# Kernel tuning notes

Measured on AMD Instinct MI355X. Metric: run time of the kernel, lower is better.

Reference implementation:

```python
import jax, jax.numpy as jnp
import numpy as np

J = 8          # number of octaves
Q = 8          # wavelets per octave (first order)
T = 16384      # signal length (power of two)
B = 4          # batch size
XI_MAX = 0.35  # center frequency of the mother wavelet (cycles/sample)


def _filters():
    """Frequency-domain Morlet-like analytic filterbank + Gaussian lowpass."""
    om = np.arange(T) / T                                   # normalized freqs in [0,1)
    # first-order: J*Q log-spaced analytic bandpass filters
    k1 = np.arange(J * Q)
    xi1 = XI_MAX * 2.0 ** (-k1 / Q)                         # (N1,) center freqs
    sig1 = xi1 * (2.0 ** (1.0 / Q) - 1.0)                   # ~1/Q-octave bandwidth
    psi1 = np.exp(-((om[None, :] - xi1[:, None]) ** 2) / (2.0 * sig1[:, None] ** 2))
    # second-order: J octave-spaced (Q2=1) wider filters
    k2 = np.arange(J).astype(np.float64)
    xi2 = XI_MAX * 2.0 ** (-k2)                             # (N2,)
    sig2 = xi2 * 0.5                                        # octave bandwidth
    psi2 = np.exp(-((om[None, :] - xi2[:, None]) ** 2) / (2.0 * sig2[:, None] ** 2))
    # lowpass phi at scale 2^J (symmetric on the circle)
    d = np.minimum(om, 1.0 - om)
    sig_phi = XI_MAX * 2.0 ** (-J)
    phi = np.exp(-(d ** 2) / (2.0 * sig_phi ** 2))
    # valid second-order paths: xi2 < xi1 (equivalent of j2 > j1)
    mask = (xi2[None, :] < xi1[:, None])                    # (N1, N2) bool
    return (jnp.asarray(psi1, jnp.float32), jnp.asarray(psi2, jnp.float32),
            jnp.asarray(phi, jnp.float32), jnp.asarray(mask))


def setup_inputs() -> dict:
    key = jax.random.key(0)
    x = jax.random.normal(key, (B, 1, T), dtype=jnp.float32)
    psi1_hat, psi2_hat, phi_hat, mask = _filters()
    return {"x": x, "psi1_hat": psi1_hat, "psi2_hat": psi2_hat,
            "phi_hat": phi_hat, "mask": mask, "stride": 2 ** J}


def reference(x, psi1_hat, psi2_hat, phi_hat, mask, stride):
    # x: (B,1,T); psi1_hat: (N1,T); psi2_hat: (N2,T); phi_hat: (T,); mask: (N1,N2)
    X = jnp.fft.fft(x)                                       # (B,1,T) complex
    lp = lambda h: jnp.real(jnp.fft.ifft(h * phi_hat))[..., ::stride]  # lowpass + subsample
    # zeroth order
    S0 = lp(X)[:, :, None, :]                                # (B,1,1,T')
    # first order: bandpass -> modulus
    U1 = jnp.abs(jnp.fft.ifft(X[:, :, None, :] * psi1_hat))  # (B,1,N1,T)
    U1h = jnp.fft.fft(U1)
    S1 = lp(U1h)                                             # (B,1,N1,T')
    # second order: bandpass the first-order envelopes -> modulus
    U2 = jnp.abs(jnp.fft.ifft(U1h[:, :, :, None, :] * psi2_hat))  # (B,1,N1,N2,T)
    S2 = lp(jnp.fft.fft(U2)) * mask[None, None, :, :, None]  # (B,1,N1,N2,T')
    b, c, n1, n2, tp = S2.shape
    S2 = S2.reshape(b, c, n1 * n2, tp)
    Sx = jnp.concatenate([S0, S1, S2], axis=2)               # (B,C=1,P,T')
    # torch module: (B,C,T,F) -> (B,1,T,F*C); with C=1 this is the identity reshape
    return Sx.reshape(b, 1, Sx.shape[2], Sx.shape[3] * c)
```

## Files before the change

kernel.cpp:

```cpp
#include <hip/hip_runtime.h>
#include <math.h>

#define T_LEN   16384
#define NTH     512
#define TPRIME  64
#define NPATH   577
#define INV_T   (1.0f/16384.0f)
#define TWO_PI  6.28318530717958647692f
#define NW      640
#define NH      (NW + 1)
#define C8C     0.92387953251128675613f
#define C8S     0.38268343236508977173f

__device__ __forceinline__ int rev4(int i) {
    int r = 0;
#pragma unroll
    for (int p = 0; p < 7; ++p) { r = (r << 2) | (i & 3); i >>= 2; }
    return r;
}
__device__ __forceinline__ int IDX(int i) {
    return i ^ ((i >> 4) & 15) ^ ((i >> 8) & 15);
}
#define S6 IDX
__device__ __forceinline__ int UIDX(int n) {
    return n ^ ((n >> 5) & 31) ^ ((n >> 10) & 31);
}
__device__ __forceinline__ int US(int n) { return n ^ ((n >> 5) & 31); }

__device__ __forceinline__ void inv_bf4(float2& A0, float2& A1, float2& A2, float2& A3,
                                        float c1, float s1) {
    float sr = A0.x + A1.x + A2.x + A3.x, si = A0.y + A1.y + A2.y + A3.y;
    float tr = A0.x - A1.y - A2.x + A3.y, ti = A0.y + A1.x - A2.y - A3.x;
    float ur = A0.x - A1.x + A2.x - A3.x, ui = A0.y - A1.y + A2.y - A3.y;
    float vr = A0.x + A1.y - A2.x - A3.y, vi = A0.y - A1.x - A2.y + A3.x;
    float c2 = c1*c1 - s1*s1, s2 = 2.f*c1*s1;
    float c3 = c1*c2 - s1*s2, s3 = c1*s2 + s1*c2;
    A0 = make_float2(sr, si);
    A1 = make_float2(tr*c1 - ti*s1, tr*s1 + ti*c1);
    A2 = make_float2(ur*c2 - ui*s2, ur*s2 + ui*c2);
    A3 = make_float2(vr*c3 - vi*s3, vr*s3 + vi*c3);
}
__device__ __forceinline__ void fwd_bf4(float2& B0, float2& B1, float2& B2, float2& B3,
                                        float c1, float s1) {
    float c2 = c1*c1 - s1*s1, s2 = 2.f*c1*s1;
    float c3 = c1*c2 - s1*s2, s3 = c1*s2 + s1*c2;
    float trr = B1.x*c1 + B1.y*s1, tii = B1.y*c1 - B1.x*s1;
    float urr = B2.x*c2 + B2.y*s2, uii = B2.y*c2 - B2.x*s2;
    float vrr = B3.x*c3 + B3.y*s3, vii = B3.y*c3 - B3.x*s3;
    float s0r = B0.x, s0i = B0.y;
    B0 = make_float2(s0r + trr + urr + vrr, s0i + tii + uii + vii);
    B1 = make_float2(s0r + tii - urr - vii, s0i - trr - uii + vrr);
    B2 = make_float2(s0r - trr + urr - vrr, s0i - tii + uii - vii);
    B3 = make_float2(s0r - tii - urr + vii, s0i + trr - uii - vrr);
}

template<int Q>
__device__ __forceinline__ void inv_group16(float2* v, int jp) {
    float a0 = (float)jp * (TWO_PI / (float)(4 * Q));
    float cw, sw; __sincosf(a0, &sw, &cw);
    float c = cw, s = sw;
#pragma unroll
    for (int rp = 0; rp < 4; ++rp) {
        inv_bf4(v[rp], v[4+rp], v[8+rp], v[12+rp], c, s);
        float cn = c*C8C - s*C8S, sn = c*C8S + s*C8C;
        c = cn; s = sn;
    }
    float b0 = (float)jp * (TWO_PI / (float)Q);
    float cb, sb; __sincosf(b0, &sb, &cb);
#pragma unroll
    for (int r = 0; r < 4; ++r)
        inv_bf4(v[4*r], v[4*r+1], v[4*r+2], v[4*r+3], cb, sb);
}
template<int QA>
__device__ __forceinline__ void fwd_group16(float2* v, int jp) {
    float aA = (float)jp * (TWO_PI / (float)(4 * QA));
    float cA, sA; __sincosf(aA, &sA, &cA);
#pragma unroll
    for (int r = 0; r < 4; ++r)
        fwd_bf4(v[4*r], v[4*r+1], v[4*r+2], v[4*r+3], cA, sA);
    float aB = (float)jp * (TWO_PI / (float)(16 * QA));
    float cB, sB; __sincosf(aB, &sB, &cB);
    float c = cB, s = sB;
#pragma unroll
    for (int rp = 0; rp < 4; ++rp) {
        fwd_bf4(v[rp], v[4+rp], v[8+rp], v[12+rp], c, s);
        float cn = c*C8C - s*C8S, sn = c*C8S + s*C8C;
        c = cn; s = sn;
    }
}

template<int LQ>
__device__ void inv_pass16(float2* buf) {
    const int q = 1 << LQ, qp = q >> 2;
    __syncthreads();
#pragma unroll
    for (int it = 0; it < 2; ++it) {
        int g2 = threadIdx.x + it * NTH;
        int jp = g2 & (qp - 1);
        int base = ((g2 >> (LQ - 2)) << (LQ + 2)) | jp;
        float2 v[16];
#pragma unroll
        for (int r = 0; r < 4; ++r)
#pragma unroll
            for (int rp = 0; rp < 4; ++rp)
                v[4*r+rp] = buf[IDX(base + r*q + rp*qp)];
        inv_group16<(1 << LQ)>(v, jp);
#pragma unroll
        for (int r = 0; r < 4; ++r)
#pragma unroll
            for (int rp = 0; rp < 4; ++rp)
                buf[IDX(base + r*q + rp*qp)] = v[4*r+rp];
    }
}

__device__ void inv_pass16_g(const float2* __restrict__ src, const float* __restrict__ filt,
                             float2* buf, int clo, int chi) {
#pragma unroll 1
    for (int it = 0; it < 2; ++it) {
        int jp = threadIdx.x + it * NTH;
        float2 v[16];
#pragma unroll
        for (int r = 0; r < 4; ++r)
#pragma unroll
            for (int rp = 0; rp < 4; ++rp) {
                int ch = 4*r + rp;
                if (ch >= clo && ch <= chi) {
                    int i = jp + r*4096 + rp*1024;
                    float2 a = src[i]; float p = filt[i];
                    v[4*r+rp] = make_float2(a.x*p, a.y*p);
                } else {
                    v[4*r+rp] = make_float2(0.f, 0.f);
                }
            }
        inv_group16<4096>(v, jp);
#pragma unroll
        for (int r = 0; r < 4; ++r)
#pragma unroll
            for (int rp = 0; rp < 4; ++rp)
                buf[IDX(jp + r*4096 + rp*1024)] = v[4*r+rp];
        asm volatile("" ::: "memory");
    }
}

__device__ void mod_fwd4(float2* buf) {
    __syncthreads();
#pragma unroll
    for (int it = 0; it < 8; ++it) {
        int base = (threadIdx.x + it * NTH) << 2;
        float2 a0 = buf[IDX(base)], a1 = buf[IDX(base+1)], a2 = buf[IDX(base+2)], a3 = buf[IDX(base+3)];
        inv_bf4(a0, a1, a2, a3, 1.0f, 0.0f);
        float2 b0 = make_float2(sqrtf(a0.x*a0.x + a0.y*a0.y) * INV_T, 0.f);
        float2 b1 = make_float2(sqrtf(a1.x*a1.x + a1.y*a1.y) * INV_T, 0.f);
        float2 b2 = make_float2(sqrtf(a2.x*a2.x + a2.y*a2.y) * INV_T, 0.f);
        float2 b3 = make_float2(sqrtf(a3.x*a3.x + a3.y*a3.y) * INV_T, 0.f);
        fwd_bf4(b0, b1, b2, b3, 1.0f, 0.0f);
        buf[IDX(base)] = b0; buf[IDX(base+1)] = b1; buf[IDX(base+2)] = b2; buf[IDX(base+3)] = b3;
    }
}

template<int LQA>
__device__ void fwd_pass16(float2* buf) {
    const int qA = 1 << LQA, qB = 4 * qA;
    __syncthreads();
#pragma unroll
    for (int it = 0; it < 2; ++it) {
        int g2 = threadIdx.x + it * NTH;
        int jp = g2 & (qA - 1);
        int base = ((g2 >> LQA) << (LQA + 4)) | jp;
        float2 v[16];
#pragma unroll
        for (int r = 0; r < 4; ++r)
#pragma unroll
            for (int rp = 0; rp < 4; ++rp)
                v[4*r+rp] = buf[IDX(base + r*qB + rp*qA)];
        fwd_group16<(1 << LQA)>(v, jp);
#pragma unroll
        for (int r = 0; r < 4; ++r)
#pragma unroll
            for (int rp = 0; rp < 4; ++rp)
                buf[IDX(base + r*qB + rp*qA)] = v[4*r+rp];
    }
}

__device__ void fwd_last_store_zs(float2* buf, float2* __restrict__ gout, int nchunks,
                                  float2* zs) {
    __syncthreads();
#pragma unroll 1
    for (int it = 0; it < 2; ++it) {
        int jp = threadIdx.x + it * NTH;
        float2 v[16];
#pragma unroll
        for (int r = 0; r < 4; ++r)
#pragma unroll
            for (int rp = 0; rp < 4; ++rp)
                v[4*r+rp] = buf[IDX(jp + r*4096 + rp*1024)];
        fwd_group16<1024>(v, jp);
        if (it == 0 && jp < 124) zs[jp] = v[0];
#pragma unroll
        for (int r = 0; r < 4; ++r)
#pragma unroll
            for (int rp = 0; rp < 4; ++rp) {
                int ch = 4*r + rp;
                if (ch < nchunks)
                    gout[jp + r*4096 + rp*1024] = v[4*r+rp];
            }
        asm volatile("" ::: "memory");
    }
}

__global__ __launch_bounds__(512) void k1_prep(const float* __restrict__ x,
                                               const float* __restrict__ phi,
                                               float2* __restrict__ Z,
                                               float* __restrict__ hws,
                                               int B2) {
    const int bi = blockIdx.x;
    if (bi < B2) {
        const int b = bi >> 1;
        const int jp = ((bi & 1) << 9) | threadIdx.x;
        const float* xb = x + (size_t)b * T_LEN;
        float2* Zb = Z + (size_t)b * T_LEN;
        float2 v[16];
#pragma unroll
        for (int r = 0; r < 4; ++r)
#pragma unroll
            for (int rp = 0; rp < 4; ++rp)
                v[4*r+rp] = make_float2(xb[jp + r*4096 + rp*1024], 0.f);
        inv_group16<4096>(v, jp);
#pragma unroll
        for (int r = 0; r < 4; ++r)
#pragma unroll
            for (int rp = 0; rp < 4; ++rp)
                Zb[jp + r*4096 + rp*1024] = v[4*r+rp];
    } else {
        const int d = (bi - B2) * 8 + (threadIdx.x >> 6);
        const int l = threadIdx.x & 63;
        float p = 0.f;
#pragma unroll
        for (int j = 0; j < 8; ++j) {
            int w = l + 64 * j;
            int k = (w < 256) ? w : (15872 + w);
            int r = (k * d) & (T_LEN - 1);
            p += phi[k] * __cosf((float)r * (TWO_PI / (float)T_LEN));
        }
        p += __shfl_xor(p, 1);  p += __shfl_xor(p, 2);  p += __shfl_xor(p, 4);
        p += __shfl_xor(p, 8);  p += __shfl_xor(p, 16); p += __shfl_xor(p, 32);
        if (l == 0 && d <= NW) hws[d] = p * INV_T;
    }
}

__global__ __launch_bounds__(256) void k2_chunk_s0(const float2* __restrict__ Z,
                                                   const float* __restrict__ x,
                                                   const float* __restrict__ hws,
                                                   float2* __restrict__ wsX,
                                                   float* __restrict__ out,
                                                   int B4) {
    __shared__ float2 lds[4096];
    __shared__ float hl[NH];
    const int bi = blockIdx.x;
    if (bi < B4) {
        const int b = bi >> 2;
        const int c0 = (bi & 3) << 12;
        const float2* Zb = Z + (size_t)b * T_LEN + c0;
        for (int i = threadIdx.x; i < 4096; i += 256) lds[IDX(i)] = Zb[i];
        {
            __syncthreads();
            int g = threadIdx.x;
            int jp = g & 63, base = ((g >> 6) << 10) | jp;
            float2 v[16];
#pragma unroll
            for (int r = 0; r < 4; ++r)
#pragma unroll
                for (int rp = 0; rp < 4; ++rp)
                    v[4*r+rp] = lds[IDX(base + r*256 + rp*64)];
            inv_group16<256>(v, jp);
#pragma unroll
            for (int r = 0; r < 4; ++r)
#pragma unroll
                for (int rp = 0; rp < 4; ++rp)
                    lds[IDX(base + r*256 + rp*64)] = v[4*r+rp];
        }
        {
            __syncthreads();
            int g = threadIdx.x;
            int jp = g & 3, base = ((g >> 2) << 6) | jp;
            float2 v[16];
#pragma unroll
            for (int r = 0; r < 4; ++r)
#pragma unroll
                for (int rp = 0; rp < 4; ++rp)
                    v[4*r+rp] = lds[IDX(base + r*16 + rp*4)];
            inv_group16<16>(v, jp);
#pragma unroll
            for (int r = 0; r < 4; ++r)
#pragma unroll
                for (int rp = 0; rp < 4; ++rp)
                    lds[IDX(base + r*16 + rp*4)] = v[4*r+rp];
        }
        __syncthreads();
        float2* W = wsX + (size_t)b * T_LEN;
#pragma unroll
        for (int it = 0; it < 4; ++it) {
            int bl = (threadIdx.x + it * 256) << 2;
            float2 a0 = lds[IDX(bl)], a1 = lds[IDX(bl+1)], a2 = lds[IDX(bl+2)], a3 = lds[IDX(bl+3)];
            inv_bf4(a0, a1, a2, a3, 1.0f, 0.0f);
            int rb = rev4(c0 + bl);
            W[rb]         = make_float2(a0.x, -a0.y);
            W[rb + 4096]  = make_float2(a1.x, -a1.y);
            W[rb + 8192]  = make_float2(a2.x, -a2.y);
            W[rb + 12288] = make_float2(a3.x, -a3.y);
        }
    } else {
        const int q = bi - B4;
        const int b = q >> 3;
        const int m0 = (q & 7) << 3;
        for (int i = threadIdx.x; i < NH; i += 256) hl[i] = hws[i];
        __syncthreads();
        const float* xb = x + (size_t)b * T_LEN;
        const int m = m0 + (threadIdx.x >> 5);
        const int s = threadIdx.x & 31;
        const int c = m << 8;
        float acc = 0.f;
        for (int e = -NW + s; e <= NW; e += 32) {
            int n = (c + e) & (T_LEN - 1);
            int a = e < 0 ? -e : e;
            acc += hl[a] * xb[n];
        }
        acc += __shfl_xor(acc, 1);  acc += __shfl_xor(acc, 2);
        acc += __shfl_xor(acc, 4);  acc += __shfl_xor(acc, 8);
        acc += __shfl_xor(acc, 16);
        if (s == 0) out[(size_t)b * (NPATH * TPRIME) + m] = acc;
    }
}

__global__ __launch_bounds__(NTH)
__attribute__((amdgpu_waves_per_eu(1, 2)))
void pass_b(const float2* __restrict__ wsX,
            const float* __restrict__ psi1,
            const float* __restrict__ phi,
            float2* __restrict__ wsU,
            float* __restrict__ out) {
    __shared__ float2 buf[T_LEN];
    __shared__ float2 zs[128];
    const int blk = blockIdx.x;
    const int b = blk >> 6, n1 = blk & 63;
    float xi1T = 5734.4f * exp2f(-(float)n1 / 8.0f);
    int clo = (int)(0.40f * xi1T) >> 10;
    int chi = ((int)(1.60f * xi1T)) >> 10; if (chi > 15) chi = 15;
    inv_pass16_g(wsX + (size_t)b * T_LEN, psi1 + (size_t)n1 * T_LEN, buf, clo, chi);
    inv_pass16<8>(buf);
    inv_pass16<4>(buf);
    mod_fwd4(buf);
    fwd_pass16<2>(buf);
    fwd_pass16<6>(buf);
    const int n2min = (n1 >> 3) + 1;
    int nch = 0;
    if (n2min <= 7) {
        int S = 24084 >> n2min;
        nch = (S >> 10) + 1; if (nch > 10) nch = 10;
    }
    fwd_last_store_zs(buf, wsU + (size_t)blk * T_LEN, nch, zs);
    __syncthreads();
    const int m = threadIdx.x >> 3;
    const int s = threadIdx.x & 7;
    float acc = 0.f;
    for (int k = 1 + s; k < 124; k += 8) {
        float ph = phi[k];
        float2 z = zs[k];
        float ang = (float)((k * m) & 63) * (TWO_PI / 64.0f);
        float sn, cs; __sincosf(ang, &sn, &cs);
        acc += 2.0f * ph * (z.x * cs - z.y * sn);
    }
    acc += __shfl_xor(acc, 1);
    acc += __shfl_xor(acc, 2);
    acc += __shfl_xor(acc, 4);
    if (s == 0) {
        acc += zs[0].x * phi[0];
        out[(size_t)b * (NPATH * TPRIME) + (size_t)(1 + n1) * TPRIME + m] = acc * INV_T;
    }
}

__global__ __launch_bounds__(256) void k4_med_zero(const float2* __restrict__ wsU,
                                                   const float* __restrict__ psi2,
                                                   const float* __restrict__ hws,
                                                   float* __restrict__ out) {
    __shared__ float2 sc[4096];
    __shared__ float u8s[8192];
    __shared__ float h2s[321];
    const int tj = threadIdx.x;
    const int idx = blockIdx.x % 312, b = blockIdx.x / 312;

    if (idx >= 24) {
        int z = idx - 24;
        int g = 0, cum = 0;
#pragma unroll
        for (int gg = 0; gg < 8; ++gg) {
            int c = 8 * (gg + 1);
            if (z >= cum + c) { cum += c; g = gg + 1; }
        }
        int zz = z - cum;
        int n1 = g * 8 + zz / (g + 1);
        int n2 = zz % (g + 1);
        if (tj < TPRIME)
            out[(size_t)b * (NPATH * TPRIME) + (size_t)(65 + (n1 << 3) + n2) * TPRIME + tj] = 0.f;
        return;
    }

    const int n2 = (idx < 8) ? 1 : 2;
    const int n1 = (idx < 8) ? idx : idx - 8;
    for (int i = tj; i < 321; i += 256) h2s[i] = 2.0f * hws[2 * i];
    const float2* Ub = wsU + (size_t)((b << 6) | n1) * T_LEN;
    const float* p2 = psi2 + (size_t)n2 * T_LEN;
    const int lim = (n2 == 1) ? 10240 : 6144;
#pragma unroll 1
    for (int h = 0; h < 2; ++h) {
        float2 v[16];
#pragma unroll
        for (int r = 0; r < 4; ++r) {
#pragma unroll
            for (int rp = 0; rp < 4; ++rp) {
                int i = tj + r*1024 + rp*256;
                float2 y0 = Ub[i]; float q0 = p2[i];
                float ar = y0.x * q0, ai = y0.y * q0;
                if (i + 4096 < lim) {
                    float2 y1 = Ub[i + 4096]; float q1 = p2[i + 4096];
                    if (h == 0) { ar += y1.x*q1; ai += y1.y*q1; }
                    else        { ar -= y1.x*q1; ai -= y1.y*q1; }
                }
                if (i + 8192 < lim) {
                    float2 y2 = Ub[i + 8192]; float q2 = p2[i + 8192];
                    ar += y2.x*q2; ai += y2.y*q2;
                }
                if (h == 1) {
                    float ang = (float)i * (TWO_PI / 8192.0f);
                    float sn, cs; __sincosf(ang, &sn, &cs);
                    float nr = ar*cs - ai*sn, ni = ar*sn + ai*cs;
                    ar = nr; ai = ni;
                }
                v[4*r+rp] = make_float2(ar, ai);
            }
            asm volatile("" ::: "memory");
        }
        inv_group16<1024>(v, tj);
#pragma unroll
        for (int r = 0; r < 4; ++r)
#pragma unroll
            for (int rp = 0; rp < 4; ++rp)
                sc[S6(tj + r*1024 + rp*256)] = v[4*r+rp];
        __syncthreads();
        {
            int jp = tj & 15, base = ((tj >> 4) << 8) | jp;
#pragma unroll
            for (int r = 0; r < 4; ++r)
#pragma unroll
                for (int rp = 0; rp < 4; ++rp)
                    v[4*r+rp] = sc[S6(base + r*64 + rp*16)];
            inv_group16<64>(v, jp);
#pragma unroll
            for (int r = 0; r < 4; ++r)
#pragma unroll
                for (int rp = 0; rp < 4; ++rp)
                    sc[S6(base + r*64 + rp*16)] = v[4*r+rp];
        }
        __syncthreads();
        float mg[16];
        {
            int base = tj << 4;
#pragma unroll
            for (int r = 0; r < 4; ++r)
#pragma unroll
                for (int rp = 0; rp < 4; ++rp)
                    v[4*r+rp] = sc[S6(base + 4*r + rp)];
            inv_group16<4>(v, 0);
#pragma unroll
            for (int k = 0; k < 16; ++k)
                mg[k] = sqrtf(v[k].x*v[k].x + v[k].y*v[k].y) * INV_T;
        }
        __syncthreads();
        int rt = ((tj & 3) << 6) | (((tj >> 2) & 3) << 4) | (((tj >> 4) & 3) << 2) | (tj >> 6);
#pragma unroll
        for (int r = 0; r < 4; ++r)
#pragma unroll
            for (int rp = 0; rp < 4; ++rp)
                u8s[UIDX(2 * (rp*1024 + r*256 + rt) + h)] = mg[4*r+rp];
    }
    __syncthreads();
    const int m = tj >> 2, s = tj & 3;
    float acc = 0.f;
    for (int e = -320 + s; e <= 320; e += 4) {
        int n = (128*m + e) & 8191;
        int a = e < 0 ? -e : e;
        acc += h2s[a] * u8s[UIDX(n)];
    }
    acc += __shfl_xor(acc, 1);
    acc += __shfl_xor(acc, 2);
    if (s == 0)
        out[(size_t)b * (NPATH * TPRIME) + (size_t)(65 + (n1 << 3) + n2) * TPRIME + m] = acc;
}

__global__ __launch_bounds__(256) void k4_small(const float2* __restrict__ wsU,
                                                const float* __restrict__ psi2,
                                                const float* __restrict__ hws,
                                                float* __restrict__ out) {
    __shared__ float2 buf[4096];
    __shared__ float hd[161];
    const int t = threadIdx.x;
    const int p = blockIdx.x % 200, b = blockIdx.x / 200;
    int n1, n2;
    if      (p < 24)  { n2 = 3; n1 = p; }
    else if (p < 56)  { n2 = 4; n1 = p - 24; }
    else if (p < 96)  { n2 = 5; n1 = p - 56; }
    else if (p < 144) { n2 = 6; n1 = p - 96; }
    else              { n2 = 7; n1 = p - 144; }
    if (t < 161) hd[t] = 4.0f * hws[4 * t];
    const int kc = ((((int)(24084.0f * exp2f(-(float)n2))) >> 10) + 1) << 2;
    const float2* Ub = wsU + (size_t)((b << 6) | n1) * T_LEN;
    const float* p2 = psi2 + (size_t)n2 * T_LEN;
    float2 v[16];
#pragma unroll
    for (int r = 0; r < 4; ++r)
#pragma unroll
        for (int rp = 0; rp < 4; ++rp) {
            int ch = 4*r + rp;
            if (ch < kc) {
                int i = t + r*1024 + rp*256;
                float2 u = Ub[i]; float pp = p2[i];
                v[4*r+rp] = make_float2(u.x*pp, u.y*pp);
            } else {
                v[4*r+rp] = make_float2(0.f, 0.f);
            }
        }
    inv_group16<1024>(v, t);
#pragma unroll
    for (int r = 0; r < 4; ++r)
#pragma unroll
        for (int rp = 0; rp < 4; ++rp)
            buf[S6(t + r*1024 + rp*256)] = v[4*r+rp];
    __syncthreads();
    {
        int jp = t & 15, base = ((t >> 4) << 8) | jp;
#pragma unroll
        for (int r = 0; r < 4; ++r)
#pragma unroll
            for (int rp = 0; rp < 4; ++rp)
                v[4*r+rp] = buf[S6(base + r*64 + rp*16)];
        inv_group16<64>(v, jp);
#pragma unroll
        for (int r = 0; r < 4; ++r)
#pragma unroll
            for (int rp = 0; rp < 4; ++rp)
                buf[S6(base + r*64 + rp*16)] = v[4*r+rp];
    }
    __syncthreads();
    float mg[16];
    {
        int base = t << 4;
#pragma unroll
        for (int r = 0; r < 4; ++r)
#pragma unroll
            for (int rp = 0; rp < 4; ++rp)
                v[4*r+rp] = buf[S6(base + 4*r + rp)];
        inv_group16<4>(v, 0);
#pragma unroll
        for (int k = 0; k < 16; ++k)
            mg[k] = sqrtf(v[k].x*v[k].x + v[k].y*v[k].y) * INV_T;
    }
    __syncthreads();
    float* uf = (float*)buf;
    int rt = ((t & 3) << 6) | (((t >> 2) & 3) << 4) | (((t >> 4) & 3) << 2) | (t >> 6);
#pragma unroll
    for (int r = 0; r < 4; ++r)
#pragma unroll
        for (int rp = 0; rp < 4; ++rp)
            uf[US(rp*1024 + r*256 + rt)] = mg[4*r+rp];
    __syncthreads();
    const int m = t >> 2, s = t & 3;
    float acc = 0.f;
    for (int e = -160 + s; e <= 160; e += 4) {
        int n = (64*m + e) & 4095;
        int a = e < 0 ? -e : e;
        acc += hd[a] * uf[US(n)];
    }
    acc += __shfl_xor(acc, 1);
    acc += __shfl_xor(acc, 2);
    if (s == 0)
        out[(size_t)b * (NPATH * TPRIME) + (size_t)(65 + (n1 << 3) + n2) * TPRIME + m] = acc;
}

extern "C" void kernel_launch(void* const* d_in, const int* in_sizes, int n_in,
                              void* d_out, int out_size, void* d_ws, size_t ws_size,
                              hipStream_t stream) {
    const float* x    = (const float*)d_in[0];
    const float* psi1 = (const float*)d_in[1];
    const float* psi2 = (const float*)d_in[2];
    const float* phi  = (const float*)d_in[3];
    float* out = (float*)d_out;

    const int B = in_sizes[0] / T_LEN;

    float*  hws = (float*)d_ws;
    float2* wsX = (float2*)((char*)d_ws + 4096);
    float2* wsU = (float2*)((char*)d_ws + 4096 + (size_t)B * T_LEN * sizeof(float2));
    float2* Z   = wsU;

    k1_prep<<<2 * B + 81, 512, 0, stream>>>(x, phi, Z, hws, 2 * B);
    k2_chunk_s0<<<4 * B + 8 * B, 256, 0, stream>>>(Z, x, hws, wsX, out, 4 * B);
    pass_b<<<B * 64, NTH, 0, stream>>>(wsX, psi1, phi, wsU, out);
    k4_med_zero<<<B * 312, 256, 0, stream>>>(wsU, psi2, hws, out);
    k4_small<<<B * 200, 256, 0, stream>>>(wsU, psi2, hws, out);
}
```

Measured before the change: 103.4 us.

## Run both half-transforms of medium paths concurrently and move zero-fill into small kernel

The medium second-order kernel now uses 512 threads per block, with two 256-thread halves computing the even and odd half-size inverse FFTs in parallel instead of looping over them sequentially. Both halves share one 64 KB shared buffer that is reused for the envelope before the lowpass reduction, which is now split eight ways per output. The zero-fill of masked-out paths is moved from the medium kernel into the small-path kernel, so the medium launch only has its 24 working blocks per batch. This aims to shorten the critical path of the few long medium blocks, at the cost of more shared memory per block and lower occupancy.

```diff
diff --git a/kernel.cpp b/kernel.cpp
--- a/kernel.cpp
+++ b/kernel.cpp
@@ -379,120 +379,105 @@
     }
 }
 
-__global__ __launch_bounds__(256) void k4_med_zero(const float2* __restrict__ wsU,
-                                                   const float* __restrict__ psi2,
-                                                   const float* __restrict__ hws,
-                                                   float* __restrict__ out) {
-    __shared__ float2 sc[4096];
-    __shared__ float u8s[8192];
+__global__ __launch_bounds__(512) void k4_med2(const float2* __restrict__ wsU,
+                                               const float* __restrict__ psi2,
+                                               const float* __restrict__ hws,
+                                               float* __restrict__ out) {
+    __shared__ float2 sc2[8192];
     __shared__ float h2s[321];
     const int tj = threadIdx.x;
-    const int idx = blockIdx.x % 312, b = blockIdx.x / 312;
-
-    if (idx >= 24) {
-        int z = idx - 24;
-        int g = 0, cum = 0;
-#pragma unroll
-        for (int gg = 0; gg < 8; ++gg) {
-            int c = 8 * (gg + 1);
-            if (z >= cum + c) { cum += c; g = gg + 1; }
-        }
-        int zz = z - cum;
-        int n1 = g * 8 + zz / (g + 1);
-        int n2 = zz % (g + 1);
-        if (tj < TPRIME)
-            out[(size_t)b * (NPATH * TPRIME) + (size_t)(65 + (n1 << 3) + n2) * TPRIME + tj] = 0.f;
-        return;
-    }
-
+    const int hh = tj >> 8, t = tj & 255;
+    const int idx = blockIdx.x % 24, b = blockIdx.x / 24;
     const int n2 = (idx < 8) ? 1 : 2;
     const int n1 = (idx < 8) ? idx : idx - 8;
-    for (int i = tj; i < 321; i += 256) h2s[i] = 2.0f * hws[2 * i];
+    for (int i = tj; i < 321; i += 512) h2s[i] = 2.0f * hws[2 * i];
+    float2* sc = sc2 + (hh << 12);
     const float2* Ub = wsU + (size_t)((b << 6) | n1) * T_LEN;
     const float* p2 = psi2 + (size_t)n2 * T_LEN;
     const int lim = (n2 == 1) ? 10240 : 6144;
-#pragma unroll 1
-    for (int h = 0; h < 2; ++h) {
-        float2 v[16];
-#pragma unroll
-        for (int r = 0; r < 4; ++r) {
-#pragma unroll
-            for (int rp = 0; rp < 4; ++rp) {
-                int i = tj + r*1024 + rp*256;
-                float2 y0 = Ub[i]; float q0 = p2[i];
-                float ar = y0.x * q0, ai = y0.y * q0;
-                if (i + 4096 < lim) {
-                    float2 y1 = Ub[i + 4096]; float q1 = p2[i + 4096];
-                    if (h == 0) { ar += y1.x*q1; ai += y1.y*q1; }
-                    else        { ar -= y1.x*q1; ai -= y1.y*q1; }
-                }
-                if (i + 8192 < lim) {
-                    float2 y2 = Ub[i + 8192]; float q2 = p2[i + 8192];
-                    ar += y2.x*q2; ai += y2.y*q2;
-                }
-                if (h == 1) {
-                    float ang = (float)i * (TWO_PI / 8192.0f);
-                    float sn, cs; __sincosf(ang, &sn, &cs);
-                    float nr = ar*cs - ai*sn, ni = ar*sn + ai*cs;
-                    ar = nr; ai = ni;
-                }
-                v[4*r+rp] = make_float2(ar, ai);
+    float2 v[16];
+#pragma unroll
+    for (int r = 0; r < 4; ++r) {
+#pragma unroll
+        for (int rp = 0; rp < 4; ++rp) {
+            int i = t + r*1024 + rp*256;
+            float2 y0 = Ub[i]; float q0 = p2[i];
+            float ar = y0.x * q0, ai = y0.y * q0;
+            if (i + 4096 < lim) {
+                float2 y1 = Ub[i + 4096]; float q1 = p2[i + 4096];
+                if (hh == 0) { ar += y1.x*q1; ai += y1.y*q1; }
+                else         { ar -= y1.x*q1; ai -= y1.y*q1; }
             }
-            asm volatile("" ::: "memory");
-        }
-        inv_group16<1024>(v, tj);
-#pragma unroll
-        for (int r = 0; r < 4; ++r)
-#pragma unroll
-            for (int rp = 0; rp < 4; ++rp)
-                sc[S6(tj + r*1024 + rp*256)] = v[4*r+rp];
-        __syncthreads();
-        {
-            int jp = tj & 15, base = ((tj >> 4) << 8) | jp;
-#pragma unroll
-            for (int r = 0; r < 4; ++r)
-#pragma unroll
-                for (int rp = 0; rp < 4; ++rp)
-                    v[4*r+rp] = sc[S6(base + r*64 + rp*16)];
-            inv_group16<64>(v, jp);
-#pragma unroll
-            for (int r = 0; r < 4; ++r)
-#pragma unroll
-                for (int rp = 0; rp < 4; ++rp)
-                    sc[S6(base + r*64 + rp*16)] = v[4*r+rp];
-        }
-        __syncthreads();
-        float mg[16];
-        {
-            int base = tj << 4;
-#pragma unroll
-            for (int r = 0; r < 4; ++r)
-#pragma unroll
-                for (int rp = 0; rp < 4; ++rp)
-                    v[4*r+rp] = sc[S6(base + 4*r + rp)];
-            inv_group16<4>(v, 0);
-#pragma unroll
-            for (int k = 0; k < 16; ++k)
-                mg[k] = sqrtf(v[k].x*v[k].x + v[k].y*v[k].y) * INV_T;
-        }
-        __syncthreads();
-        int rt = ((tj & 3) << 6) | (((tj >> 2) & 3) << 4) | (((tj >> 4) & 3) << 2) | (tj >> 6);
-#pragma unroll
-        for (int r = 0; r < 4; ++r)
-#pragma unroll
-            for (int rp = 0; rp < 4; ++rp)
-                u8s[UIDX(2 * (rp*1024 + r*256 + rt) + h)] = mg[4*r+rp];
-    }
-    __syncthreads();
-    const int m = tj >> 2, s = tj & 3;
+            if (i + 8192 < lim) {
+                float2 y2 = Ub[i + 8192]; float q2 = p2[i + 8192];
+                ar += y2.x*q2; ai += y2.y*q2;
+            }
+            if (hh == 1) {
+                float ang = (float)i * (TWO_PI / 8192.0f);
+                float sn, cs; __sincosf(ang, &sn, &cs);
+                float nr = ar*cs - ai*sn, ni = ar*sn + ai*cs;
+                ar = nr; ai = ni;
+            }
+            v[4*r+rp] = make_float2(ar, ai);
+        }
+        asm volatile("" ::: "memory");
+    }
+    inv_group16<1024>(v, t);
+#pragma unroll
+    for (int r = 0; r < 4; ++r)
+#pragma unroll
+        for (int rp = 0; rp < 4; ++rp)
+            sc[S6(t + r*1024 + rp*256)] = v[4*r+rp];
+    __syncthreads();
+    {
+        int jp = t & 15, base = ((t >> 4) << 8) | jp;
+#pragma unroll
+        for (int r = 0; r < 4; ++r)
+#pragma unroll
+            for (int rp = 0; rp < 4; ++rp)
+                v[4*r+rp] = sc[S6(base + r*64 + rp*16)];
+        inv_group16<64>(v, jp);
+#pragma unroll
+        for (int r = 0; r < 4; ++r)
+#pragma unroll
+            for (int rp = 0; rp < 4; ++rp)
+                sc[S6(base + r*64 + rp*16)] = v[4*r+rp];
+    }
+    __syncthreads();
+    float mg[16];
+    {
+        int base = t << 4;
+#pragma unroll
+        for (int r = 0; r < 4; ++r)
+#pragma unroll
+            for (int rp = 0; rp < 4; ++rp)
+                v[4*r+rp] = sc[S6(base + 4*r + rp)];
+        inv_group16<4>(v, 0);
+#pragma unroll
+        for (int k = 0; k < 16; ++k)
+            mg[k] = sqrtf(v[k].x*v[k].x + v[k].y*v[k].y) * INV_T;
+    }
+    __syncthreads();
+    float* u8s = (float*)sc2;
+    int rt = ((t & 3) << 6) | (((t >> 2) & 3) << 4) | (((t >> 4) & 3) << 2) | (t >> 6);
+#pragma unroll
+    for (int r = 0; r < 4; ++r)
+#pragma unroll
+        for (int rp = 0; rp < 4; ++rp) {
+            int pos = rp*1024 + r*256 + rt;
+            u8s[UIDX(2 * pos + hh)] = mg[4*r+rp];
+        }
+    __syncthreads();
+    const int m = tj >> 3, s = tj & 7;
     float acc = 0.f;
-    for (int e = -320 + s; e <= 320; e += 4) {
+    for (int e = -320 + s; e <= 320; e += 8) {
         int n = (128*m + e) & 8191;
         int a = e < 0 ? -e : e;
         acc += h2s[a] * u8s[UIDX(n)];
     }
     acc += __shfl_xor(acc, 1);
     acc += __shfl_xor(acc, 2);
+    acc += __shfl_xor(acc, 4);
     if (s == 0)
         out[(size_t)b * (NPATH * TPRIME) + (size_t)(65 + (n1 << 3) + n2) * TPRIME + m] = acc;
 }
@@ -504,7 +489,25 @@
     __shared__ float2 buf[4096];
     __shared__ float hd[161];
     const int t = threadIdx.x;
-    const int p = blockIdx.x % 200, b = blockIdx.x / 200;
+    const int idx = blockIdx.x % 488, b = blockIdx.x / 488;
+
+    if (idx >= 200) {
+        int z = idx - 200;
+        int g = 0, cum = 0;
+#pragma unroll
+        for (int gg = 0; gg < 8; ++gg) {
+            int c = 8 * (gg + 1);
+            if (z >= cum + c) { cum += c; g = gg + 1; }
+        }
+        int zz = z - cum;
+        int n1 = g * 8 + zz / (g + 1);
+        int n2 = zz % (g + 1);
+        if (t < TPRIME)
+            out[(size_t)b * (NPATH * TPRIME) + (size_t)(65 + (n1 << 3) + n2) * TPRIME + t] = 0.f;
+        return;
+    }
+
+    const int p = idx;
     int n1, n2;
     if      (p < 24)  { n2 = 3; n1 = p; }
     else if (p < 56)  { n2 = 4; n1 = p - 24; }
@@ -605,6 +608,6 @@
     k1_prep<<<2 * B + 81, 512, 0, stream>>>(x, phi, Z, hws, 2 * B);
     k2_chunk_s0<<<4 * B + 8 * B, 256, 0, stream>>>(Z, x, hws, wsX, out, 4 * B);
     pass_b<<<B * 64, NTH, 0, stream>>>(wsX, psi1, phi, wsU, out);
-    k4_med_zero<<<B * 312, 256, 0, stream>>>(wsU, psi2, hws, out);
-    k4_small<<<B * 200, 256, 0, stream>>>(wsU, psi2, hws, out);
-}
+    k4_med2<<<B * 24, 512, 0, stream>>>(wsU, psi2, hws, out);
+    k4_small<<<B * 488, 256, 0, stream>>>(wsU, psi2, hws, out);
+}
```

New measurement: 91.49 us (median of 2 runs). -11.5%, faster.
